# Kernel optimization log

Measured on AMD Instinct MI355X. Metric: run time of the kernel, lower is better.

## Reference

```python
import jax, jax.numpy as jnp
import numpy as np

B, T, C, H = 4, 1024, 2048, 16
D = C // H  # head dim = 128
ALPHA_Q, BETA_Q = -128, 127


def _quant_params(w):
    # symmetric range per tensor, as in get_symmetric_range/get_tensor_quantization_parameters
    beta = float(np.abs(w).max())
    alpha = -beta
    s = (beta - alpha) / (BETA_Q - ALPHA_Q)
    z = int((beta * ALPHA_Q - alpha * BETA_Q) / (beta - alpha))
    return s, z


def _quantize(w, s, z):
    return np.clip(np.round(w / s + z), ALPHA_Q, BETA_Q).astype(np.int8)


def setup_inputs() -> dict:
    key = jax.random.key(0)
    x = jax.random.normal(key, (B, T, C), dtype=jnp.float32)
    rng = np.random.default_rng(0)
    # fp32 master weights (GPT init scale), then quantize per-tensor symmetric int8
    params = {
        'w_attn': rng.normal(0.0, 0.02, (3 * C, C)).astype(np.float32),
        'b_attn': rng.normal(0.0, 0.02, (3 * C,)).astype(np.float32),
        'w_proj': rng.normal(0.0, 0.02, (C, C)).astype(np.float32),
        'b_proj': rng.normal(0.0, 0.02, (C,)).astype(np.float32),
    }
    out = {'x': x}
    for name, arr in params.items():
        s, z = _quant_params(arr)
        out[name + '_q'] = jnp.asarray(_quantize(arr, s, z))
        out['s_' + name] = jnp.float32(s)
        out['z_' + name] = z  # python int, zero-point constant
    return out


def _dequant(wq, s, z):
    # dequantize_tensor: s * (int8 -> int32 - z) -> float32
    return s * (wq.astype(jnp.int32) - z).astype(jnp.float32)


def reference(x, w_attn_q, s_w_attn, z_w_attn, b_attn_q, s_b_attn, z_b_attn,
              w_proj_q, s_w_proj, z_w_proj, b_proj_q, s_b_proj, z_b_proj):
    wa = _dequant(w_attn_q, s_w_attn, z_w_attn)   # [3C, C]
    ba = _dequant(b_attn_q, s_b_attn, z_b_attn)   # [3C]
    wp = _dequant(w_proj_q, s_w_proj, z_w_proj)   # [C, C]
    bp = _dequant(b_proj_q, s_b_proj, z_b_proj)   # [C]

    qkv = jnp.einsum('btc,oc->bto', x, wa) + ba   # [B,T,3C]
    q, k, v = jnp.split(qkv, 3, axis=-1)
    # [B,T,C] -> [B,H,T,D]
    q = q.reshape(B, T, H, D).transpose(0, 2, 1, 3)
    k = k.reshape(B, T, H, D).transpose(0, 2, 1, 3)
    v = v.reshape(B, T, H, D).transpose(0, 2, 1, 3)

    scale = 1.0 / jnp.sqrt(jnp.float32(D))
    scores = jnp.einsum('bhqd,bhkd->bhqk', q, k) * scale  # [B,H,T,T]
    causal = jnp.tril(jnp.ones((T, T), dtype=bool))
    scores = jnp.where(causal, scores, jnp.finfo(scores.dtype).min)
    att = jax.nn.softmax(scores, axis=-1)
    y = jnp.einsum('bhqk,bhkd->bhqd', att, v)      # [B,H,T,D]
    y = y.transpose(0, 2, 1, 3).reshape(B, T, C)

    return jnp.einsum('btc,oc->bto', y, wp) + bp   # [B,T,C]
```

## Files before the change

kernel.cpp:

```cpp
#include <hip/hip_runtime.h>
#include <stdint.h>
#include <math.h>

typedef unsigned short u16;
typedef __attribute__((ext_vector_type(4))) float f32x4;
typedef __attribute__((ext_vector_type(4))) int i32x4;
typedef __attribute__((ext_vector_type(8))) short bf16x8;

__device__ __forceinline__ u16 f2bf(float f) {
  uint32_t u = __float_as_uint(f);
  u += 0x7FFFu + ((u >> 16) & 1u);
  return (u16)(u >> 16);
}

__device__ __forceinline__ void async16(const void* g, void* l) {
  __builtin_amdgcn_global_load_lds(
      (const __attribute__((address_space(1))) void*)g,
      (__attribute__((address_space(3))) void*)l, 16, 0, 0);
}

__global__ void prep_fused(
    const float4* __restrict__ x, char4* __restrict__ xq, float* __restrict__ srow,
    const int4* __restrict__ waq, char4* __restrict__ wa8, const int* __restrict__ z_wa,
    const int4* __restrict__ wpq, ushort4* __restrict__ wp_bf,
    const float* __restrict__ s_wp, const int* __restrict__ z_wp) {
  __shared__ float red[4];
  const int bid = blockIdx.x;
  const int tid = threadIdx.x;
  if (bid < 4096) {
    const int row = bid;
    const int i0 = row * 512 + tid * 2;
    float4 v0 = x[i0];
    float4 v1 = x[i0 + 1];
    float m = fmaxf(fmaxf(fmaxf(fabsf(v0.x), fabsf(v0.y)), fmaxf(fabsf(v0.z), fabsf(v0.w))),
                    fmaxf(fmaxf(fabsf(v1.x), fabsf(v1.y)), fmaxf(fabsf(v1.z), fabsf(v1.w))));
#pragma unroll
    for (int s = 1; s < 64; s <<= 1) m = fmaxf(m, __shfl_xor(m, s));
    if ((tid & 63) == 0) red[tid >> 6] = m;
    __syncthreads();
    m = fmaxf(fmaxf(red[0], red[1]), fmaxf(red[2], red[3]));
    const float inv = 127.0f / m;
    char4 r0, r1;
    r0.x = (char)__float2int_rn(v0.x * inv);
    r0.y = (char)__float2int_rn(v0.y * inv);
    r0.z = (char)__float2int_rn(v0.z * inv);
    r0.w = (char)__float2int_rn(v0.w * inv);
    r1.x = (char)__float2int_rn(v1.x * inv);
    r1.y = (char)__float2int_rn(v1.y * inv);
    r1.z = (char)__float2int_rn(v1.z * inv);
    r1.w = (char)__float2int_rn(v1.w * inv);
    xq[i0] = r0;
    xq[i0 + 1] = r1;
    if (tid == 0) srow[row] = m * (1.0f / 127.0f);
  } else if (bid < 16384) {
    const int zv = z_wa[0];
    const int i = (bid - 4096) * 256 + tid;
    int4 v = waq[i];
    char4 r;
    r.x = (char)(v.x - zv); r.y = (char)(v.y - zv);
    r.z = (char)(v.z - zv); r.w = (char)(v.w - zv);
    wa8[i] = r;
  } else {
    const float sv = s_wp[0];
    const int zv = z_wp[0];
    const int i = (bid - 16384) * 256 + tid;
    int4 v = wpq[i];
    ushort4 r;
    r.x = f2bf(sv * (float)(v.x - zv));
    r.y = f2bf(sv * (float)(v.y - zv));
    r.z = f2bf(sv * (float)(v.z - zv));
    r.w = f2bf(sv * (float)(v.w - zv));
    wp_bf[i] = r;
  }
}

__global__ __launch_bounds__(256, 4) void gemm_i8_qkv(
    const char* __restrict__ A, const char* __restrict__ B, int K,
    const float* __restrict__ sw, const float* __restrict__ srow,
    const int* __restrict__ bq, const float* __restrict__ bs, const int* __restrict__ bz,
    u16* __restrict__ qb, u16* __restrict__ kb, u16* __restrict__ vT) {
  __shared__ uint8_t sA[16384];
  __shared__ uint8_t sB[16384];
  const int tid = threadIdx.x;
  const int wave = tid >> 6, lane = tid & 63;
  const int quad = lane >> 4, l16 = lane & 15;
  const int wm = wave >> 1, wn = wave & 1;
  const int Mb = blockIdx.y << 7, Nb = blockIdx.x << 7;

  const char* ag[4];
  const char* bg[4];
  int lo[4];
#pragma unroll
  for (int i = 0; i < 4; ++i) {
    int row = wave * 32 + i * 8 + (lane >> 3);
    int c = (lane & 7) ^ (row & 7);
    ag[i] = A + (size_t)(Mb + row) * K + c * 16;
    bg[i] = B + (size_t)(Nb + row) * K + c * 16;
    lo[i] = wave * 4096 + i * 1024 + lane * 16;
  }

  i32x4 acc[4][4] = {};

  for (int kk = 0; kk < K; kk += 128) {
    __syncthreads();
#pragma unroll
    for (int i = 0; i < 4; ++i) {
      async16(ag[i] + kk, sA + lo[i]);
      async16(bg[i] + kk, sB + lo[i]);
    }
    __syncthreads();
#pragma unroll
    for (int ks = 0; ks < 2; ++ks) {
      i32x4 af[4], bfr[4];
#pragma unroll
      for (int t = 0; t < 4; ++t) {
        int m = wm * 64 + t * 16 + l16;
        af[t] = *(const i32x4*)(sA + m * 128 + ((((ks << 2) + quad) ^ (m & 7)) << 4));
        int n = wn * 64 + t * 16 + l16;
        bfr[t] = *(const i32x4*)(sB + n * 128 + ((((ks << 2) + quad) ^ (n & 7)) << 4));
      }
#pragma unroll
      for (int mt = 0; mt < 4; ++mt)
#pragma unroll
        for (int nt = 0; nt < 4; ++nt)
          acc[mt][nt] = __builtin_amdgcn_mfma_i32_16x16x64_i8(af[mt], bfr[nt], acc[mt][nt], 0, 0, 0);
    }
  }

  const float swa = sw[0];
  float svr[4][4];
#pragma unroll
  for (int mt = 0; mt < 4; ++mt) {
    const int m0 = Mb + wm * 64 + mt * 16 + quad * 4;
#pragma unroll
    for (int r = 0; r < 4; ++r) svr[mt][r] = swa * srow[m0 + r];
  }
  const float sbv = bs[0];
  const int zbv = bz[0];
#pragma unroll
  for (int nt = 0; nt < 4; ++nt) {
    const int o = Nb + wn * 64 + nt * 16 + l16;
    const float bias = sbv * (float)(bq[o] - zbv);
    const int which = o >> 11;
    const int cc = o & 2047;
    const int h = cc >> 7, d = cc & 127;
#pragma unroll
    for (int mt = 0; mt < 4; ++mt) {
      const int m0 = Mb + wm * 64 + mt * 16 + quad * 4;
      const int bi = m0 >> 10, t0 = m0 & 1023;
      const size_t bhx = (size_t)bi * 16 + h;
      if (which == 2) {
        ushort4 pv;
        pv.x = f2bf((float)acc[mt][nt][0] * svr[mt][0] + bias);
        pv.y = f2bf((float)acc[mt][nt][1] * svr[mt][1] + bias);
        pv.z = f2bf((float)acc[mt][nt][2] * svr[mt][2] + bias);
        pv.w = f2bf((float)acc[mt][nt][3] * svr[mt][3] + bias);
        *(ushort4*)(vT + (bhx * 128 + d) * 1024 + t0) = pv;
      } else {
        u16* dst = (which == 0 ? qb : kb) + (bhx * 1024 + t0) * 128 + d;
#pragma unroll
        for (int r = 0; r < 4; ++r)
          dst[r * 128] = f2bf((float)acc[mt][nt][r] * svr[mt][r] + bias);
      }
    }
  }
}

__global__ __launch_bounds__(256, 4) void gemm_bt_out(
    const u16* __restrict__ A, const u16* __restrict__ B, int K, int N,
    const int* __restrict__ bq, const float* __restrict__ bs, const int* __restrict__ bz,
    float* __restrict__ out) {
  __shared__ uint8_t sA[16384];
  __shared__ uint8_t sB[16384];
  const int tid = threadIdx.x;
  const int wave = tid >> 6, lane = tid & 63;
  const int quad = lane >> 4, l16 = lane & 15;
  const int wm = wave >> 1, wn = wave & 1;
  const int Mb = blockIdx.y << 7, Nb = blockIdx.x << 7;

  const u16* ag[4];
  const u16* bg[4];
  int lo[4];
#pragma unroll
  for (int i = 0; i < 4; ++i) {
    int row = wave * 32 + i * 8 + (lane >> 3);
    int c = (lane & 7) ^ (row & 7);
    ag[i] = A + (size_t)(Mb + row) * K + c * 8;
    bg[i] = B + (size_t)(Nb + row) * K + c * 8;
    lo[i] = wave * 4096 + i * 1024 + lane * 16;
  }

  f32x4 acc[4][4] = {};

  for (int kk = 0; kk < K; kk += 64) {
    __syncthreads();
#pragma unroll
    for (int i = 0; i < 4; ++i) {
      async16(ag[i] + kk, sA + lo[i]);
      async16(bg[i] + kk, sB + lo[i]);
    }
    __syncthreads();
#pragma unroll
    for (int ks = 0; ks < 2; ++ks) {
      bf16x8 af[4], bfr[4];
#pragma unroll
      for (int t = 0; t < 4; ++t) {
        int m = wm * 64 + t * 16 + l16;
        af[t] = *(const bf16x8*)(sA + m * 128 + ((((ks << 2) + quad) ^ (m & 7)) << 4));
        int n = wn * 64 + t * 16 + l16;
        bfr[t] = *(const bf16x8*)(sB + n * 128 + ((((ks << 2) + quad) ^ (n & 7)) << 4));
      }
#pragma unroll
      for (int mt = 0; mt < 4; ++mt)
#pragma unroll
        for (int nt = 0; nt < 4; ++nt)
          acc[mt][nt] = __builtin_amdgcn_mfma_f32_16x16x32_bf16(af[mt], bfr[nt], acc[mt][nt], 0, 0, 0);
    }
  }

  const float sbv = bs[0];
  const int zbv = bz[0];
#pragma unroll
  for (int nt = 0; nt < 4; ++nt) {
    const int o = Nb + wn * 64 + nt * 16 + l16;
    const float bias = sbv * (float)(bq[o] - zbv);
#pragma unroll
    for (int mt = 0; mt < 4; ++mt) {
      const int m0 = Mb + wm * 64 + mt * 16 + quad * 4;
#pragma unroll
      for (int r = 0; r < 4; ++r)
        out[(size_t)(m0 + r) * N + o] = acc[mt][nt][r] + bias;
    }
  }
}

__global__ __launch_bounds__(256, 2) void attn_fwd(
    const u16* __restrict__ qg, const u16* __restrict__ kg,
    const u16* __restrict__ vg, u16* __restrict__ yb) {
  __shared__ uint8_t smem[81920];
  uint8_t* sVb = smem + 32768;
  uint8_t* sP = smem + 65536;
  const int tid = threadIdx.x;
  const int wave = tid >> 6, lane = tid & 63;
  const int quad = lane >> 4, l16 = lane & 15;
  const int bh = blockIdx.x;
  const int y = blockIdx.y;
  const int qi = (y < 4) ? (7 - y) : (y - 4);
  const int qbase = qi << 7;
  const size_t base = (size_t)bh << 17;
  const u16* Q = qg + base;
  const u16* Kp = kg + base;
  const u16* Vp = vg + base;

#pragma unroll
  for (int i = 0; i < 8; ++i) {
    int off = wave * 8192 + i * 1024;
    int row = (off >> 8) + quad;
    int c = l16 ^ (row & 15);
    async16(Q + (size_t)(qbase + row) * 128 + c * 8, smem + off + lane * 16);
  }
  __syncthreads();
  bf16x8 qf[2][4];
#pragma unroll
  for (int mi = 0; mi < 2; ++mi)
#pragma unroll
    for (int ks = 0; ks < 4; ++ks) {
      int m = wave * 32 + mi * 16 + l16;
      qf[mi][ks] = *(const bf16x8*)(smem + m * 256 + ((((ks << 2) + quad) ^ (m & 15)) << 4));
    }
  asm volatile("s_waitcnt lgkmcnt(0)" ::: "memory");
  __builtin_amdgcn_sched_barrier(0);
  __builtin_amdgcn_s_barrier();

#define STAGEKV(TB, SL) do {                                                  \
    _Pragma("unroll")                                                         \
    for (int i_ = 0; i_ < 4; ++i_) {                                          \
      int off_ = wave * 4096 + i_ * 1024;                                     \
      int rowk_ = (off_ >> 8) + quad;                                         \
      int ck_ = l16 ^ (rowk_ & 15);                                           \
      async16(Kp + (size_t)((TB) + rowk_) * 128 + ck_ * 8,                    \
              smem + (SL) * 16384 + off_ + lane * 16);                        \
      int rowd_ = (off_ >> 7) + (lane >> 3);                                  \
      int cv_ = (lane & 7) ^ (rowd_ & 7);                                     \
      async16(Vp + (size_t)rowd_ * 1024 + (TB) + cv_ * 8,                     \
              sVb + (SL) * 16384 + off_ + lane * 16);                         \
    }                                                                         \
  } while (0)

  f32x4 accO[2][8] = {};
  float lacc[2][4] = {};

  const float scale = 0.088388347648318447f;
  const int jmax = 2 * qi + 1;

  STAGEKV(0, 0);

  for (int j = 0; j <= jmax; ++j) {
    const int tb = j << 6;
    const int jn = (j + 1 <= jmax) ? j + 1 : jmax;
    STAGEKV(jn << 6, (j + 1) & 1);
    asm volatile("s_waitcnt vmcnt(8)" ::: "memory");
    __builtin_amdgcn_s_barrier();
    const uint8_t* sK = smem + (j & 1) * 16384;
    const uint8_t* sV = sVb + (j & 1) * 16384;

    f32x4 sc[2][4] = {};
#pragma unroll
    for (int ks = 0; ks < 4; ++ks) {
      bf16x8 kf[4];
#pragma unroll
      for (int ni = 0; ni < 4; ++ni) {
        int n = ni * 16 + l16;
        kf[ni] = *(const bf16x8*)(sK + n * 256 + ((((ks << 2) + quad) ^ (n & 15)) << 4));
      }
#pragma unroll
      for (int mi = 0; mi < 2; ++mi)
#pragma unroll
        for (int ni = 0; ni < 4; ++ni)
          sc[mi][ni] = __builtin_amdgcn_mfma_f32_16x16x32_bf16(qf[mi][ks], kf[ni], sc[mi][ni], 0, 0, 0);
    }

    const bool needmask = (tb + 63) > qbase;
#pragma unroll
    for (int mi = 0; mi < 2; ++mi) {
      const int row0 = qbase + wave * 32 + mi * 16 + quad * 4;
#pragma unroll
      for (int ni = 0; ni < 4; ++ni) {
        const int col = tb + ni * 16 + l16;
#pragma unroll
        for (int r = 0; r < 4; ++r) {
          float s = sc[mi][ni][r] * scale;
          if (needmask && col > row0 + r) s = -INFINITY;
          float p = __expf(s);
          sc[mi][ni][r] = p;
          lacc[mi][r] += p;
        }
      }
    }

#pragma unroll
    for (int mi = 0; mi < 2; ++mi)
#pragma unroll
      for (int ni = 0; ni < 4; ++ni)
#pragma unroll
        for (int r = 0; r < 4; ++r) {
          int qr = wave * 32 + mi * 16 + quad * 4 + r;
          int kc = ni * 16 + l16;
          *(u16*)(sP + qr * 128 + (((kc >> 3) ^ (qr & 7)) << 4) + (kc & 7) * 2) =
              f2bf(sc[mi][ni][r]);
        }

#pragma unroll
    for (int ks = 0; ks < 2; ++ks) {
      bf16x8 pf[2], vf[8];
#pragma unroll
      for (int mi = 0; mi < 2; ++mi) {
        int m = wave * 32 + mi * 16 + l16;
        pf[mi] = *(const bf16x8*)(sP + m * 128 + ((((ks << 2) + quad) ^ (m & 7)) << 4));
      }
#pragma unroll
      for (int ni = 0; ni < 8; ++ni) {
        int n = ni * 16 + l16;
        vf[ni] = *(const bf16x8*)(sV + n * 128 + ((((ks << 2) + quad) ^ (n & 7)) << 4));
      }
#pragma unroll
      for (int mi = 0; mi < 2; ++mi)
#pragma unroll
        for (int ni = 0; ni < 8; ++ni)
          accO[mi][ni] = __builtin_amdgcn_mfma_f32_16x16x32_bf16(pf[mi], vf[ni], accO[mi][ni], 0, 0, 0);
    }
    __builtin_amdgcn_s_barrier();
  }
  asm volatile("s_waitcnt vmcnt(0)" ::: "memory");

  const int b = bh >> 4, h = bh & 15;
#pragma unroll
  for (int mi = 0; mi < 2; ++mi) {
    float inv[4];
#pragma unroll
    for (int r = 0; r < 4; ++r) {
      float l = lacc[mi][r];
#pragma unroll
      for (int x = 1; x < 16; x <<= 1) l += __shfl_xor(l, x);
      inv[r] = 1.0f / l;
    }
#pragma unroll
    for (int ni = 0; ni < 8; ++ni)
#pragma unroll
      for (int r = 0; r < 4; ++r) {
        int row = qbase + wave * 32 + mi * 16 + quad * 4 + r;
        int col = (h << 7) + ni * 16 + l16;
        yb[((size_t)(b * 1024 + row) << 11) + col] = f2bf(accO[mi][ni][r] * inv[r]);
      }
  }
#undef STAGEKV
}

extern "C" void kernel_launch(void* const* d_in, const int* in_sizes, int n_in,
                              void* d_out, int out_size, void* d_ws, size_t ws_size,
                              hipStream_t stream) {
  const float* x = (const float*)d_in[0];
  const int* waq = (const int*)d_in[1];
  const float* s_wa = (const float*)d_in[2];
  const int* z_wa = (const int*)d_in[3];
  const int* baq = (const int*)d_in[4];
  const float* s_ba = (const float*)d_in[5];
  const int* z_ba = (const int*)d_in[6];
  const int* wpq = (const int*)d_in[7];
  const float* s_wp = (const float*)d_in[8];
  const int* z_wp = (const int*)d_in[9];
  const int* bpq = (const int*)d_in[10];
  const float* s_bp = (const float*)d_in[11];
  const int* z_bp = (const int*)d_in[12];

  char* ws = (char*)d_ws;
  char* xq    = ws + 0;
  char* wa8   = ws + 8388608;
  u16* wp_bf  = (u16*)(ws + 20971520);
  u16* qb     = (u16*)(ws + 29360128);
  u16* kb     = (u16*)(ws + 46137344);
  u16* vT     = (u16*)(ws + 62914560);
  u16* yb     = (u16*)(ws + 79691776);
  float* srow = (float*)(ws + 96468992);

  prep_fused<<<20480, 256, 0, stream>>>(
      (const float4*)x, (char4*)xq, srow,
      (const int4*)waq, (char4*)wa8, z_wa,
      (const int4*)wpq, (ushort4*)wp_bf, s_wp, z_wp);

  gemm_i8_qkv<<<dim3(48, 32), 256, 0, stream>>>(xq, wa8, 2048, s_wa, srow,
                                                baq, s_ba, z_ba, qb, kb, vT);

  attn_fwd<<<dim3(64, 8), 256, 0, stream>>>(qb, kb, vT, yb);

  gemm_bt_out<<<dim3(16, 32), 256, 0, stream>>>(yb, wp_bf, 2048, 2048,
                                                bpq, s_bp, z_bp, (float*)d_out);
}
```

Before: 290.6 us.

## Shrink attention query tile to 64 rows and drop K/V double buffering

The attention kernel now handles 64 query rows per block instead of 128 and launches twice as many blocks. LDS use falls from 80KB to 40KB and the launch-bounds occupancy hint rises from 2 to 4 blocks per CU. The K/V double-buffered async prefetch is replaced by single-buffered loads with __syncthreads around each tile, so memory latency is now hidden by occupancy rather than by software pipelining. Each K/V tile is reused by half as many query rows, which increases total K/V traffic.

```diff
diff --git a/kernel.cpp b/kernel.cpp
--- a/kernel.cpp
+++ b/kernel.cpp
@@ -234,77 +234,61 @@
   }
 }
 
-__global__ __launch_bounds__(256, 2) void attn_fwd(
+__global__ __launch_bounds__(256, 4) void attn_fwd(
     const u16* __restrict__ qg, const u16* __restrict__ kg,
     const u16* __restrict__ vg, u16* __restrict__ yb) {
-  __shared__ uint8_t smem[81920];
-  uint8_t* sVb = smem + 32768;
-  uint8_t* sP = smem + 65536;
+  __shared__ uint8_t smem[40960];
+  uint8_t* sK = smem;
+  uint8_t* sV = smem + 16384;
+  uint8_t* sP = smem + 32768;
   const int tid = threadIdx.x;
   const int wave = tid >> 6, lane = tid & 63;
   const int quad = lane >> 4, l16 = lane & 15;
   const int bh = blockIdx.x;
   const int y = blockIdx.y;
-  const int qi = (y < 4) ? (7 - y) : (y - 4);
-  const int qbase = qi << 7;
+  const int qi = (y < 8) ? (15 - y) : (y - 8);
+  const int qbase = qi << 6;
   const size_t base = (size_t)bh << 17;
   const u16* Q = qg + base;
   const u16* Kp = kg + base;
   const u16* Vp = vg + base;
 
 #pragma unroll
-  for (int i = 0; i < 8; ++i) {
-    int off = wave * 8192 + i * 1024;
+  for (int i = 0; i < 4; ++i) {
+    int off = wave * 4096 + i * 1024;
     int row = (off >> 8) + quad;
     int c = l16 ^ (row & 15);
-    async16(Q + (size_t)(qbase + row) * 128 + c * 8, smem + off + lane * 16);
+    async16(Q + (size_t)(qbase + row) * 128 + c * 8, sK + off + lane * 16);
   }
   __syncthreads();
-  bf16x8 qf[2][4];
-#pragma unroll
-  for (int mi = 0; mi < 2; ++mi)
-#pragma unroll
-    for (int ks = 0; ks < 4; ++ks) {
-      int m = wave * 32 + mi * 16 + l16;
-      qf[mi][ks] = *(const bf16x8*)(smem + m * 256 + ((((ks << 2) + quad) ^ (m & 15)) << 4));
-    }
-  asm volatile("s_waitcnt lgkmcnt(0)" ::: "memory");
-  __builtin_amdgcn_sched_barrier(0);
-  __builtin_amdgcn_s_barrier();
-
-#define STAGEKV(TB, SL) do {                                                  \
-    _Pragma("unroll")                                                         \
-    for (int i_ = 0; i_ < 4; ++i_) {                                          \
-      int off_ = wave * 4096 + i_ * 1024;                                     \
-      int rowk_ = (off_ >> 8) + quad;                                         \
-      int ck_ = l16 ^ (rowk_ & 15);                                           \
-      async16(Kp + (size_t)((TB) + rowk_) * 128 + ck_ * 8,                    \
-              smem + (SL) * 16384 + off_ + lane * 16);                        \
-      int rowd_ = (off_ >> 7) + (lane >> 3);                                  \
-      int cv_ = (lane & 7) ^ (rowd_ & 7);                                     \
-      async16(Vp + (size_t)rowd_ * 1024 + (TB) + cv_ * 8,                     \
-              sVb + (SL) * 16384 + off_ + lane * 16);                         \
-    }                                                                         \
-  } while (0)
-
-  f32x4 accO[2][8] = {};
-  float lacc[2][4] = {};
-
+  bf16x8 qf[4];
+#pragma unroll
+  for (int ks = 0; ks < 4; ++ks) {
+    int m = wave * 16 + l16;
+    qf[ks] = *(const bf16x8*)(sK + m * 256 + ((((ks << 2) + quad) ^ (m & 15)) << 4));
+  }
+
+  f32x4 accO[8] = {};
+  float lacc[4] = {};
   const float scale = 0.088388347648318447f;
-  const int jmax = 2 * qi + 1;
-
-  STAGEKV(0, 0);
+  const int jmax = qi;
 
   for (int j = 0; j <= jmax; ++j) {
     const int tb = j << 6;
-    const int jn = (j + 1 <= jmax) ? j + 1 : jmax;
-    STAGEKV(jn << 6, (j + 1) & 1);
-    asm volatile("s_waitcnt vmcnt(8)" ::: "memory");
-    __builtin_amdgcn_s_barrier();
-    const uint8_t* sK = smem + (j & 1) * 16384;
-    const uint8_t* sV = sVb + (j & 1) * 16384;
-
-    f32x4 sc[2][4] = {};
+    __syncthreads();
+#pragma unroll
+    for (int i = 0; i < 4; ++i) {
+      int off = wave * 4096 + i * 1024;
+      int rowk = (off >> 8) + quad;
+      int ck = l16 ^ (rowk & 15);
+      async16(Kp + (size_t)(tb + rowk) * 128 + ck * 8, sK + off + lane * 16);
+      int rowd = (off >> 7) + (lane >> 3);
+      int cv = (lane & 7) ^ (rowd & 7);
+      async16(Vp + (size_t)rowd * 1024 + tb + cv * 8, sV + off + lane * 16);
+    }
+    __syncthreads();
+
+    f32x4 sc[4] = {};
 #pragma unroll
     for (int ks = 0; ks < 4; ++ks) {
       bf16x8 kf[4];
@@ -314,86 +298,68 @@
         kf[ni] = *(const bf16x8*)(sK + n * 256 + ((((ks << 2) + quad) ^ (n & 15)) << 4));
       }
 #pragma unroll
-      for (int mi = 0; mi < 2; ++mi)
-#pragma unroll
-        for (int ni = 0; ni < 4; ++ni)
-          sc[mi][ni] = __builtin_amdgcn_mfma_f32_16x16x32_bf16(qf[mi][ks], kf[ni], sc[mi][ni], 0, 0, 0);
+      for (int ni = 0; ni < 4; ++ni)
+        sc[ni] = __builtin_amdgcn_mfma_f32_16x16x32_bf16(qf[ks], kf[ni], sc[ni], 0, 0, 0);
     }
 
     const bool needmask = (tb + 63) > qbase;
-#pragma unroll
-    for (int mi = 0; mi < 2; ++mi) {
-      const int row0 = qbase + wave * 32 + mi * 16 + quad * 4;
-#pragma unroll
-      for (int ni = 0; ni < 4; ++ni) {
-        const int col = tb + ni * 16 + l16;
-#pragma unroll
-        for (int r = 0; r < 4; ++r) {
-          float s = sc[mi][ni][r] * scale;
-          if (needmask && col > row0 + r) s = -INFINITY;
-          float p = __expf(s);
-          sc[mi][ni][r] = p;
-          lacc[mi][r] += p;
-        }
-      }
-    }
-
-#pragma unroll
-    for (int mi = 0; mi < 2; ++mi)
-#pragma unroll
-      for (int ni = 0; ni < 4; ++ni)
-#pragma unroll
-        for (int r = 0; r < 4; ++r) {
-          int qr = wave * 32 + mi * 16 + quad * 4 + r;
-          int kc = ni * 16 + l16;
-          *(u16*)(sP + qr * 128 + (((kc >> 3) ^ (qr & 7)) << 4) + (kc & 7) * 2) =
-              f2bf(sc[mi][ni][r]);
-        }
+    const int row0 = qbase + wave * 16 + quad * 4;
+#pragma unroll
+    for (int ni = 0; ni < 4; ++ni) {
+      const int col = tb + ni * 16 + l16;
+#pragma unroll
+      for (int r = 0; r < 4; ++r) {
+        float s = sc[ni][r] * scale;
+        if (needmask && col > row0 + r) s = -INFINITY;
+        float p = __expf(s);
+        sc[ni][r] = p;
+        lacc[r] += p;
+      }
+    }
+
+#pragma unroll
+    for (int ni = 0; ni < 4; ++ni)
+#pragma unroll
+      for (int r = 0; r < 4; ++r) {
+        int qr = wave * 16 + quad * 4 + r;
+        int kc = ni * 16 + l16;
+        *(u16*)(sP + qr * 128 + (((kc >> 3) ^ (qr & 7)) << 4) + (kc & 7) * 2) =
+            f2bf(sc[ni][r]);
+      }
 
 #pragma unroll
     for (int ks = 0; ks < 2; ++ks) {
-      bf16x8 pf[2], vf[8];
-#pragma unroll
-      for (int mi = 0; mi < 2; ++mi) {
-        int m = wave * 32 + mi * 16 + l16;
-        pf[mi] = *(const bf16x8*)(sP + m * 128 + ((((ks << 2) + quad) ^ (m & 7)) << 4));
-      }
+      bf16x8 pf, vf[8];
+      int m = wave * 16 + l16;
+      pf = *(const bf16x8*)(sP + m * 128 + ((((ks << 2) + quad) ^ (m & 7)) << 4));
 #pragma unroll
       for (int ni = 0; ni < 8; ++ni) {
         int n = ni * 16 + l16;
         vf[ni] = *(const bf16x8*)(sV + n * 128 + ((((ks << 2) + quad) ^ (n & 7)) << 4));
       }
 #pragma unroll
-      for (int mi = 0; mi < 2; ++mi)
-#pragma unroll
-        for (int ni = 0; ni < 8; ++ni)
-          accO[mi][ni] = __builtin_amdgcn_mfma_f32_16x16x32_bf16(pf[mi], vf[ni], accO[mi][ni], 0, 0, 0);
-    }
-    __builtin_amdgcn_s_barrier();
-  }
-  asm volatile("s_waitcnt vmcnt(0)" ::: "memory");
+      for (int ni = 0; ni < 8; ++ni)
+        accO[ni] = __builtin_amdgcn_mfma_f32_16x16x32_bf16(pf, vf[ni], accO[ni], 0, 0, 0);
+    }
+  }
 
   const int b = bh >> 4, h = bh & 15;
-#pragma unroll
-  for (int mi = 0; mi < 2; ++mi) {
-    float inv[4];
+  float inv[4];
+#pragma unroll
+  for (int r = 0; r < 4; ++r) {
+    float l = lacc[r];
+#pragma unroll
+    for (int xw = 1; xw < 16; xw <<= 1) l += __shfl_xor(l, xw);
+    inv[r] = 1.0f / l;
+  }
+#pragma unroll
+  for (int ni = 0; ni < 8; ++ni)
 #pragma unroll
     for (int r = 0; r < 4; ++r) {
-      float l = lacc[mi][r];
-#pragma unroll
-      for (int x = 1; x < 16; x <<= 1) l += __shfl_xor(l, x);
-      inv[r] = 1.0f / l;
-    }
-#pragma unroll
-    for (int ni = 0; ni < 8; ++ni)
-#pragma unroll
-      for (int r = 0; r < 4; ++r) {
-        int row = qbase + wave * 32 + mi * 16 + quad * 4 + r;
-        int col = (h << 7) + ni * 16 + l16;
-        yb[((size_t)(b * 1024 + row) << 11) + col] = f2bf(accO[mi][ni][r] * inv[r]);
-      }
-  }
-#undef STAGEKV
+      int row = qbase + wave * 16 + quad * 4 + r;
+      int col = (h << 7) + ni * 16 + l16;
+      yb[((size_t)(b * 1024 + row) << 11) + col] = f2bf(accO[ni][r] * inv[r]);
+    }
 }
 
 extern "C" void kernel_launch(void* const* d_in, const int* in_sizes, int n_in,
@@ -431,7 +397,7 @@
   gemm_i8_qkv<<<dim3(48, 32), 256, 0, stream>>>(xq, wa8, 2048, s_wa, srow,
                                                 baq, s_ba, z_ba, qb, kb, vT);
 
-  attn_fwd<<<dim3(64, 8), 256, 0, stream>>>(qb, kb, vT, yb);
+  attn_fwd<<<dim3(64, 16), 256, 0, stream>>>(qb, kb, vT, yb);
 
   gemm_bt_out<<<dim3(16, 32), 256, 0, stream>>>(yb, wp_bf, 2048, 2048,
                                                 bpq, s_bp, z_bp, (float*)d_out);
```

After: 295.7 us. About the same (+1.7%).

## Drop K/V double buffering in attention to fit three blocks per CU

Applied to the files above, without the earlier changes.

The attention kernel goes from double-buffered K/V tiles (80KB LDS, prefetch of the next tile overlapped with compute) to a single buffer (48KB LDS) loaded synchronously each iteration between two __syncthreads. Launch bounds rise from 2 to 3 blocks per CU. The goal is to hide memory latency through higher occupancy instead of software pipelining. In exchange, every tile load is now exposed inside each block, and the tighter register budget may cause spills.

```diff
diff --git a/kernel.cpp b/kernel.cpp
--- a/kernel.cpp
+++ b/kernel.cpp
@@ -234,12 +234,13 @@
   }
 }
 
-__global__ __launch_bounds__(256, 2) void attn_fwd(
+__global__ __launch_bounds__(256, 3) void attn_fwd(
     const u16* __restrict__ qg, const u16* __restrict__ kg,
     const u16* __restrict__ vg, u16* __restrict__ yb) {
-  __shared__ uint8_t smem[81920];
-  uint8_t* sVb = smem + 32768;
-  uint8_t* sP = smem + 65536;
+  __shared__ uint8_t smem[49152];
+  uint8_t* sK = smem;
+  uint8_t* sV = smem + 16384;
+  uint8_t* sP = smem + 32768;
   const int tid = threadIdx.x;
   const int wave = tid >> 6, lane = tid & 63;
   const int quad = lane >> 4, l16 = lane & 15;
@@ -268,41 +269,26 @@
       int m = wave * 32 + mi * 16 + l16;
       qf[mi][ks] = *(const bf16x8*)(smem + m * 256 + ((((ks << 2) + quad) ^ (m & 15)) << 4));
     }
-  asm volatile("s_waitcnt lgkmcnt(0)" ::: "memory");
-  __builtin_amdgcn_sched_barrier(0);
-  __builtin_amdgcn_s_barrier();
-
-#define STAGEKV(TB, SL) do {                                                  \
-    _Pragma("unroll")                                                         \
-    for (int i_ = 0; i_ < 4; ++i_) {                                          \
-      int off_ = wave * 4096 + i_ * 1024;                                     \
-      int rowk_ = (off_ >> 8) + quad;                                         \
-      int ck_ = l16 ^ (rowk_ & 15);                                           \
-      async16(Kp + (size_t)((TB) + rowk_) * 128 + ck_ * 8,                    \
-              smem + (SL) * 16384 + off_ + lane * 16);                        \
-      int rowd_ = (off_ >> 7) + (lane >> 3);                                  \
-      int cv_ = (lane & 7) ^ (rowd_ & 7);                                     \
-      async16(Vp + (size_t)rowd_ * 1024 + (TB) + cv_ * 8,                     \
-              sVb + (SL) * 16384 + off_ + lane * 16);                         \
-    }                                                                         \
-  } while (0)
 
   f32x4 accO[2][8] = {};
   float lacc[2][4] = {};
-
   const float scale = 0.088388347648318447f;
   const int jmax = 2 * qi + 1;
 
-  STAGEKV(0, 0);
-
   for (int j = 0; j <= jmax; ++j) {
     const int tb = j << 6;
-    const int jn = (j + 1 <= jmax) ? j + 1 : jmax;
-    STAGEKV(jn << 6, (j + 1) & 1);
-    asm volatile("s_waitcnt vmcnt(8)" ::: "memory");
-    __builtin_amdgcn_s_barrier();
-    const uint8_t* sK = smem + (j & 1) * 16384;
-    const uint8_t* sV = sVb + (j & 1) * 16384;
+    __syncthreads();
+#pragma unroll
+    for (int i = 0; i < 4; ++i) {
+      int off = wave * 4096 + i * 1024;
+      int rowk = (off >> 8) + quad;
+      int ck = l16 ^ (rowk & 15);
+      async16(Kp + (size_t)(tb + rowk) * 128 + ck * 8, sK + off + lane * 16);
+      int rowd = (off >> 7) + (lane >> 3);
+      int cv = (lane & 7) ^ (rowd & 7);
+      async16(Vp + (size_t)rowd * 1024 + tb + cv * 8, sV + off + lane * 16);
+    }
+    __syncthreads();
 
     f32x4 sc[2][4] = {};
 #pragma unroll
@@ -369,9 +355,7 @@
         for (int ni = 0; ni < 8; ++ni)
           accO[mi][ni] = __builtin_amdgcn_mfma_f32_16x16x32_bf16(pf[mi], vf[ni], accO[mi][ni], 0, 0, 0);
     }
-    __builtin_amdgcn_s_barrier();
-  }
-  asm volatile("s_waitcnt vmcnt(0)" ::: "memory");
+  }
 
   const int b = bh >> 4, h = bh & 15;
 #pragma unroll
@@ -381,7 +365,7 @@
     for (int r = 0; r < 4; ++r) {
       float l = lacc[mi][r];
 #pragma unroll
-      for (int x = 1; x < 16; x <<= 1) l += __shfl_xor(l, x);
+      for (int xw = 1; xw < 16; xw <<= 1) l += __shfl_xor(l, xw);
       inv[r] = 1.0f / l;
     }
 #pragma unroll
@@ -393,7 +377,6 @@
         yb[((size_t)(b * 1024 + row) << 11) + col] = f2bf(accO[mi][ni][r] * inv[r]);
       }
   }
-#undef STAGEKV
 }
 
 extern "C" void kernel_launch(void* const* d_in, const int* in_sizes, int n_in,
```

Measured after the change: 375.0 us. 1.29x slower.
